# Kernel tuning notes

Measured on AMD Instinct MI355X. Metric: run time of the kernel, lower is better.

The kernel has to match this reference:

```python
import jax, jax.numpy as jnp
import numpy as np


def setup_inputs() -> dict:
    key = jax.random.key(0)
    ks = jax.random.split(key, 5)
    B, S, D_IN, D_OUT, NB, R = 4, 2048, 4096, 4096, 16, 64
    bi, bo = D_IN // NB, D_OUT // NB  # 256, 256
    x = jax.random.normal(ks[0], (B, S, D_IN), dtype=jnp.float32)
    blocks = jax.random.normal(ks[1], (NB, bo, bi), dtype=jnp.float32) * 0.02
    U = jax.random.normal(ks[2], (D_OUT, R), dtype=jnp.float32) * 0.02
    V = jax.random.normal(ks[3], (D_IN, R), dtype=jnp.float32) * 0.02
    bias = jax.random.normal(ks[4], (D_OUT,), dtype=jnp.float32)
    alpha = jnp.ones((1,), dtype=jnp.float32)
    return {"x": x, "blocks": blocks, "U": U, "V": V, "bias": bias, "alpha": alpha}


def reference(x, blocks, U, V, bias, alpha):
    # y = BlockDiag(W) x + U V^T x, scaled by alpha, plus bias.
    NB, bo, bi = blocks.shape
    batch_dims = x.shape[:-1]
    in_features = x.shape[-1]
    out_features = NB * bo
    x_flat = x.reshape(-1, in_features)                 # [N, D_in]
    x_blk = x_flat.reshape(-1, NB, bi)                  # [N, nb, bi]
    # block-diagonal: per-block GEMM with block.T, batched over blocks
    y_blk = jnp.einsum('nbi,boi->nbo', x_blk, blocks)   # [N, nb, bo]
    y_blockdiag = y_blk.reshape(-1, out_features)       # [N, D_out]
    # low-rank global term: (x V) U^T
    y_lowrank = (x_flat @ V) @ U.T                      # [N, D_out]
    result = (y_blockdiag + y_lowrank) * alpha + bias
    return result.reshape(*batch_dims, out_features)
```

## Files before the change

### kernel.cpp

```cpp
#include <hip/hip_runtime.h>
#include <hip/hip_bf16.h>


typedef __attribute__((ext_vector_type(8))) short short8;
typedef __attribute__((ext_vector_type(4))) float f32x4;

#define DIN 4096
#define DOUT 4096
#define KCAT 320

static __device__ __forceinline__ short f2bf(float f) {
  return __builtin_bit_cast(short, __float2bfloat16(f));
}
static __device__ __forceinline__ unsigned short f2bfu(float f) {
  return __builtin_bit_cast(unsigned short, __float2bfloat16(f));
}
static __device__ __forceinline__ short8 pack8(f32x4 a, f32x4 b) {
  short8 r;
  r[0] = f2bf(a[0]); r[1] = f2bf(a[1]); r[2] = f2bf(a[2]); r[3] = f2bf(a[3]);
  r[4] = f2bf(b[0]); r[5] = f2bf(b[1]); r[6] = f2bf(b[2]); r[7] = f2bf(b[3]);
  return r;
}
static __device__ __forceinline__ void gload_lds16(const void* g, void* l) {
  __builtin_amdgcn_global_load_lds(
      (const __attribute__((address_space(1))) unsigned int*)g,
      (__attribute__((address_space(3))) unsigned int*)l, 16, 0, 0);
}

__global__ __launch_bounds__(256) void prep_kernel(
    const float* __restrict__ blocks, const float* __restrict__ U,
    const float* __restrict__ V, unsigned short* __restrict__ Bmat,
    unsigned short* __restrict__ VT) {
  int g = blockIdx.x * 256 + threadIdx.x;
  const int total1 = DOUT * KCAT;
  if (g < total1) {
    int o = g / KCAT;
    int k = g - o * KCAT;
    float v;
    if (k < 256)
      v = blocks[((o >> 8) << 16) | ((o & 255) << 8) | k];
    else
      v = U[o * 64 + (k - 256)];
    Bmat[g] = f2bfu(v);
  } else {
    int g2 = g - total1;
    if (g2 < 64 * DIN) {
      int r = g2 >> 12;
      int i = g2 & (DIN - 1);
      VT[g2] = f2bfu(V[i * 64 + r]);
    }
  }
}

__global__ __launch_bounds__(256) void k1_xv(const float* __restrict__ x,
                                             const unsigned short* __restrict__ VT,
                                             float* __restrict__ tpart, int nrows) {
  const int rt = blockIdx.x >> 2;
  const int kc = blockIdx.x & 3;
  const int tid = threadIdx.x;
  const int w = tid >> 6, l = tid & 63;
  const int r0 = rt * 64 + w * 16;
  const int ko = (l >> 4) << 3;
  f32x4 acc[4];
#pragma unroll
  for (int i = 0; i < 4; ++i) acc[i] = (f32x4){0.f, 0.f, 0.f, 0.f};
  const float* xp = x + (size_t)(r0 + (l & 15)) * DIN + kc * 1024 + ko;
  const unsigned short* vp[4];
#pragma unroll
  for (int ct = 0; ct < 4; ++ct)
    vp[ct] = VT + (size_t)(ct * 16 + (l & 15)) * DIN + kc * 1024 + ko;
#pragma unroll 4
  for (int k = 0; k < 1024; k += 32) {
    f32x4 v0 = *(const f32x4*)(xp + k);
    f32x4 v1 = *(const f32x4*)(xp + k + 4);
    short8 af = pack8(v0, v1);
#pragma unroll
    for (int ct = 0; ct < 4; ++ct) {
      short8 bf = *(const short8*)(vp[ct] + k);
      acc[ct] = __builtin_amdgcn_mfma_f32_16x16x32_bf16(af, bf, acc[ct], 0, 0, 0);
    }
  }
  float* tp = tpart + (size_t)kc * nrows * 64;
  const int orow = r0 + ((l >> 4) << 2);
  const int ocol = l & 15;
#pragma unroll
  for (int ct = 0; ct < 4; ++ct)
#pragma unroll
    for (int r = 0; r < 4; ++r)
      tp[(size_t)(orow + r) * 64 + ct * 16 + ocol] = acc[ct][r];
}

__global__ __launch_bounds__(256) void k1_reduce(const float* __restrict__ tpart,
                                                 float* __restrict__ tfin, int n4) {
  int i = blockIdx.x * 256 + threadIdx.x;
  if (i >= n4) return;
  const f32x4* p = (const f32x4*)tpart;
  f32x4 s = p[i] + p[i + n4] + p[i + 2 * n4] + p[i + 3 * n4];
  ((f32x4*)tfin)[i] = s;
}

__global__ __launch_bounds__(256, 3) void k2_main(
    const float* __restrict__ x, const float* __restrict__ tfin,
    const unsigned short* __restrict__ Bmat, const float* __restrict__ bias,
    const float* __restrict__ alphap, float* __restrict__ out, int nrt) {
  __shared__ __align__(1024) float ldsA[128 * 64];
  __shared__ __align__(1024) unsigned short ldsB[128 * 64];
  const int NCT = DOUT / 128;
  const int nwg = nrt * NCT;
  const int cpx = nwg >> 3;
  const int id = blockIdx.x;
  const int sw = (id & 7) * cpx + (id >> 3);
  const int rt = sw / NCT;
  const int ct = sw - rt * NCT;
  const int row0 = rt * 128, col0 = ct * 128;
  const int b = ct >> 1;
  const int tid = threadIdx.x;
  const int w = tid >> 6, l = tid & 63;
  const int wm = w >> 1, wn = w & 1;

  int offX[8], offT[8];
#pragma unroll
  for (int r2 = 0; r2 < 8; ++r2) {
    int seg = r2 * 4 + w;
    int row = seg * 4 + (l >> 4);
    int chunk = (l & 15) >> 1;
    int half = l & 1;
    int col = (((chunk ^ (row & 7)) << 3) | (((half ^ (row >> 3)) & 1) << 2));
    offX[r2] = row * DIN + col;
    offT[r2] = row * 64 + col;
  }
  size_t offB[4];
#pragma unroll
  for (int r2 = 0; r2 < 4; ++r2) {
    int seg = r2 * 4 + w;
    int n = seg * 8 + (l >> 3);
    int kk = ((l & 7) ^ (n & 7)) << 3;
    offB[r2] = (size_t)(col0 + n) * KCAT + kk;
  }
  const float* xbase = x + (size_t)row0 * DIN + b * 256;
  const float* tbase = tfin + (size_t)row0 * 64;

  f32x4 acc[4][4];
#pragma unroll
  for (int mi = 0; mi < 4; ++mi)
#pragma unroll
    for (int ni = 0; ni < 4; ++ni) acc[mi][ni] = (f32x4){0.f, 0.f, 0.f, 0.f};

  char* ldsAb = (char*)ldsA;
  char* ldsBb = (char*)ldsB;
#pragma unroll
  for (int step = 0; step < 5; ++step) {
#pragma unroll
    for (int r2 = 0; r2 < 8; ++r2) {
      const float* src = (step < 4) ? (xbase + step * 64 + offX[r2]) : (tbase + offT[r2]);
      gload_lds16(src, ldsAb + (r2 * 4 + w) * 1024);
    }
#pragma unroll
    for (int r2 = 0; r2 < 4; ++r2)
      gload_lds16(Bmat + offB[r2] + step * 64, ldsBb + (r2 * 4 + w) * 1024);
    asm volatile("s_waitcnt vmcnt(0)" ::: "memory");
    __syncthreads();
#pragma unroll
    for (int ks = 0; ks < 2; ++ks) {
      short8 af[4], bfr[4];
#pragma unroll
      for (int mi = 0; mi < 4; ++mi) {
        int row = wm * 64 + mi * 16 + (l & 15);
        int kc2 = ks * 4 + (l >> 4);
        int off = row * 256 + (((kc2 ^ (row & 7)) << 5) | (((row >> 3) & 1) << 4));
        f32x4 v0 = *(const f32x4*)(ldsAb + off);
        f32x4 v1 = *(const f32x4*)(ldsAb + (off ^ 16));
        af[mi] = pack8(v0, v1);
      }
#pragma unroll
      for (int ni = 0; ni < 4; ++ni) {
        int n = wn * 64 + ni * 16 + (l & 15);
        int kc2 = ks * 4 + (l >> 4);
        int off = n * 128 + ((kc2 ^ (n & 7)) << 4);
        bfr[ni] = *(const short8*)(ldsBb + off);
      }
#pragma unroll
      for (int mi = 0; mi < 4; ++mi)
#pragma unroll
        for (int ni = 0; ni < 4; ++ni)
          acc[mi][ni] =
              __builtin_amdgcn_mfma_f32_16x16x32_bf16(af[mi], bfr[ni], acc[mi][ni], 0, 0, 0);
    }
    __syncthreads();
  }
  const float alpha = alphap[0];
#pragma unroll
  for (int ni = 0; ni < 4; ++ni) {
    int col = col0 + wn * 64 + ni * 16 + (l & 15);
    float bs = bias[col];
#pragma unroll
    for (int mi = 0; mi < 4; ++mi) {
      int rbase = row0 + wm * 64 + mi * 16 + ((l >> 4) << 2);
#pragma unroll
      for (int r = 0; r < 4; ++r)
        out[(size_t)(rbase + r) * DOUT + col] = acc[mi][ni][r] * alpha + bs;
    }
  }
}

extern "C" void kernel_launch(void* const* d_in, const int* in_sizes, int n_in,
                              void* d_out, int out_size, void* d_ws, size_t ws_size,
                              hipStream_t stream) {
  const float* x      = (const float*)d_in[0];
  const float* blocks = (const float*)d_in[1];
  const float* U      = (const float*)d_in[2];
  const float* V      = (const float*)d_in[3];
  const float* bias   = (const float*)d_in[4];
  const float* alpha  = (const float*)d_in[5];
  float* out = (float*)d_out;
  const int nrows = in_sizes[0] / DIN;

  char* ws = (char*)d_ws;
  float* tpart = (float*)ws;
  float* tfin  = (float*)(ws + (size_t)4 * nrows * 64 * 4);
  unsigned short* Bmat =
      (unsigned short*)(ws + (size_t)5 * nrows * 64 * 4);
  unsigned short* VT =
      (unsigned short*)(ws + (size_t)5 * nrows * 64 * 4 + (size_t)DOUT * KCAT * 2);

  const int prep_blocks = (DOUT * KCAT + 64 * DIN + 255) / 256;
  prep_kernel<<<prep_blocks, 256, 0, stream>>>(blocks, U, V, Bmat, VT);
  k1_xv<<<(nrows / 64) * 4, 256, 0, stream>>>(x, VT, tpart, nrows);
  k1_reduce<<<(nrows * 64 / 4 + 255) / 256, 256, 0, stream>>>(tpart, tfin, nrows * 64 / 4);
  k2_main<<<(nrows / 128) * (DOUT / 128), 256, 0, stream>>>(x, tfin, Bmat, bias, alpha, out,
                                                            nrows / 128);
}
```

Baseline: 301.9 us.

## Double-buffer k2_main tiles and convert A to bf16 before LDS staging

Restructures the main GEMM loop into a two-stage software pipeline: the next step's B tile is fetched via global_load_lds and the next A tile into registers while the current step's MFMAs run. A is converted from fp32 to bf16 in registers before being written to LDS, which halves A's LDS footprint and removes the per-fragment conversion in the compute loop. The cost is more registers for the prefetched A values, which is why the launch bound drops to 2 waves per SIMD, lowering occupancy.

Measured after the change: 307.6 us. No clear change (+1.9%).

```diff
diff --git a/kernel.cpp b/kernel.cpp
--- a/kernel.cpp
+++ b/kernel.cpp
@@ -99,12 +99,12 @@
   ((f32x4*)tfin)[i] = s;
 }
 
-__global__ __launch_bounds__(256, 3) void k2_main(
+__global__ __launch_bounds__(256, 2) void k2_main(
     const float* __restrict__ x, const float* __restrict__ tfin,
     const unsigned short* __restrict__ Bmat, const float* __restrict__ bias,
     const float* __restrict__ alphap, float* __restrict__ out, int nrt) {
-  __shared__ __align__(1024) float ldsA[128 * 64];
-  __shared__ __align__(1024) unsigned short ldsB[128 * 64];
+  __shared__ __align__(1024) unsigned short ldsA[2][128 * 64];
+  __shared__ __align__(1024) unsigned short ldsB[2][128 * 64];
   const int NCT = DOUT / 128;
   const int nwg = nrt * NCT;
   const int cpx = nwg >> 3;
@@ -118,27 +118,19 @@
   const int w = tid >> 6, l = tid & 63;
   const int wm = w >> 1, wn = w & 1;
 
-  int offX[8], offT[8];
-#pragma unroll
-  for (int r2 = 0; r2 < 8; ++r2) {
-    int seg = r2 * 4 + w;
-    int row = seg * 4 + (l >> 4);
-    int chunk = (l & 15) >> 1;
-    int half = l & 1;
-    int col = (((chunk ^ (row & 7)) << 3) | (((half ^ (row >> 3)) & 1) << 2));
-    offX[r2] = row * DIN + col;
-    offT[r2] = row * 64 + col;
-  }
-  size_t offB[4];
+  const int rA = tid >> 3;
+  const int c8 = tid & 7;
+
+  int offB[4];
 #pragma unroll
   for (int r2 = 0; r2 < 4; ++r2) {
     int seg = r2 * 4 + w;
     int n = seg * 8 + (l >> 3);
     int kk = ((l & 7) ^ (n & 7)) << 3;
-    offB[r2] = (size_t)(col0 + n) * KCAT + kk;
-  }
-  const float* xbase = x + (size_t)row0 * DIN + b * 256;
-  const float* tbase = tfin + (size_t)row0 * 64;
+    offB[r2] = (col0 + n) * KCAT + kk;
+  }
+  const float* xcb = x + (size_t)row0 * DIN + b * 256;
+  const float* tb = tfin + (size_t)row0 * 64;
 
   f32x4 acc[4][4];
 #pragma unroll
@@ -146,48 +138,78 @@
 #pragma unroll
     for (int ni = 0; ni < 4; ++ni) acc[mi][ni] = (f32x4){0.f, 0.f, 0.f, 0.f};
 
-  char* ldsAb = (char*)ldsA;
-  char* ldsBb = (char*)ldsB;
-#pragma unroll
-  for (int step = 0; step < 5; ++step) {
-#pragma unroll
-    for (int r2 = 0; r2 < 8; ++r2) {
-      const float* src = (step < 4) ? (xbase + step * 64 + offX[r2]) : (tbase + offT[r2]);
-      gload_lds16(src, ldsAb + (r2 * 4 + w) * 1024);
-    }
-#pragma unroll
-    for (int r2 = 0; r2 < 4; ++r2)
-      gload_lds16(Bmat + offB[r2] + step * 64, ldsBb + (r2 * 4 + w) * 1024);
+  f32x4 a0[4], a1[4];
+  char* ldsAc = (char*)&ldsA[0][0];
+  char* ldsBc = (char*)&ldsB[0][0];
+
+#define ISSUE_A(s)                                                              \
+  {                                                                             \
+    _Pragma("unroll") for (int q = 0; q < 4; ++q) {                             \
+      const float* src = ((s) < 4)                                              \
+          ? (xcb + (size_t)(q * 32 + rA) * DIN + (s) * 64 + c8 * 8)             \
+          : (tb + (q * 32 + rA) * 64 + c8 * 8);                                 \
+      a0[q] = *(const f32x4*)src;                                               \
+      a1[q] = *(const f32x4*)(src + 4);                                         \
+    }                                                                           \
+  }
+#define ISSUE_B(s, buf)                                                         \
+  {                                                                             \
+    _Pragma("unroll") for (int r2 = 0; r2 < 4; ++r2)                            \
+        gload_lds16(Bmat + offB[r2] + (s) * 64,                                 \
+                    ldsBc + (buf) * 16384 + (r2 * 4 + w) * 1024);               \
+  }
+#define WRITE_A(buf)                                                            \
+  {                                                                             \
+    _Pragma("unroll") for (int q = 0; q < 4; ++q) {                             \
+      int row = q * 32 + rA;                                                    \
+      short8 p = pack8(a0[q], a1[q]);                                           \
+      *(short8*)(ldsAc + (buf) * 16384 + row * 128 + ((c8 ^ (row & 7)) << 4)) = \
+          p;                                                                    \
+    }                                                                           \
+  }
+#define COMPUTE(buf)                                                            \
+  {                                                                             \
+    _Pragma("unroll") for (int ks = 0; ks < 2; ++ks) {                          \
+      short8 af[4], bfr[4];                                                     \
+      _Pragma("unroll") for (int mi = 0; mi < 4; ++mi) {                        \
+        int row = wm * 64 + mi * 16 + (l & 15);                                 \
+        int u = (ks * 4 + (l >> 4)) ^ (row & 7);                                \
+        af[mi] = *(const short8*)(ldsAc + (buf) * 16384 + row * 128 + (u << 4));\
+      }                                                                         \
+      _Pragma("unroll") for (int ni = 0; ni < 4; ++ni) {                        \
+        int n = wn * 64 + ni * 16 + (l & 15);                                   \
+        int u = (ks * 4 + (l >> 4)) ^ (n & 7);                                  \
+        bfr[ni] = *(const short8*)(ldsBc + (buf) * 16384 + n * 128 + (u << 4)); \
+      }                                                                         \
+      _Pragma("unroll") for (int mi = 0; mi < 4; ++mi)                          \
+          _Pragma("unroll") for (int ni = 0; ni < 4; ++ni)                      \
+              acc[mi][ni] = __builtin_amdgcn_mfma_f32_16x16x32_bf16(            \
+                  af[mi], bfr[ni], acc[mi][ni], 0, 0, 0);                       \
+    }                                                                           \
+  }
+
+  ISSUE_B(0, 0);
+  ISSUE_A(0);
+  WRITE_A(0);
+  asm volatile("s_waitcnt vmcnt(0)" ::: "memory");
+  __syncthreads();
+
+#pragma unroll
+  for (int s = 0; s < 5; ++s) {
+    const int buf = s & 1;
+    if (s < 4) {
+      ISSUE_B(s + 1, buf ^ 1);
+      ISSUE_A(s + 1);
+    }
+    COMPUTE(buf);
+    if (s < 4) {
+      __builtin_amdgcn_sched_barrier(0);
+      WRITE_A(buf ^ 1);
+    }
     asm volatile("s_waitcnt vmcnt(0)" ::: "memory");
     __syncthreads();
-#pragma unroll
-    for (int ks = 0; ks < 2; ++ks) {
-      short8 af[4], bfr[4];
-#pragma unroll
-      for (int mi = 0; mi < 4; ++mi) {
-        int row = wm * 64 + mi * 16 + (l & 15);
-        int kc2 = ks * 4 + (l >> 4);
-        int off = row * 256 + (((kc2 ^ (row & 7)) << 5) | (((row >> 3) & 1) << 4));
-        f32x4 v0 = *(const f32x4*)(ldsAb + off);
-        f32x4 v1 = *(const f32x4*)(ldsAb + (off ^ 16));
-        af[mi] = pack8(v0, v1);
-      }
-#pragma unroll
-      for (int ni = 0; ni < 4; ++ni) {
-        int n = wn * 64 + ni * 16 + (l & 15);
-        int kc2 = ks * 4 + (l >> 4);
-        int off = n * 128 + ((kc2 ^ (n & 7)) << 4);
-        bfr[ni] = *(const short8*)(ldsBb + off);
-      }
-#pragma unroll
-      for (int mi = 0; mi < 4; ++mi)
-#pragma unroll
-        for (int ni = 0; ni < 4; ++ni)
-          acc[mi][ni] =
-              __builtin_amdgcn_mfma_f32_16x16x32_bf16(af[mi], bfr[ni], acc[mi][ni], 0, 0, 0);
-    }
-    __syncthreads();
-  }
+  }
+
   const float alpha = alphap[0];
 #pragma unroll
   for (int ni = 0; ni < 4; ++ni) {
@@ -201,6 +223,10 @@
         out[(size_t)(rbase + r) * DOUT + col] = acc[mi][ni][r] * alpha + bs;
     }
   }
+#undef ISSUE_A
+#undef ISSUE_B
+#undef WRITE_A
+#undef COMPUTE
 }
 
 extern "C" void kernel_launch(void* const* d_in, const int* in_sizes, int n_in,
```

## Load A operand directly from global, double-buffer B in LDS, fuse partial reduction

Applied to the files above, without the earlier changes.

Removes the k1_reduce kernel and instead sums the four split-K partials of x·V inside k2_main when forming the low-rank A fragment. The A operand (x and t) is now read straight from global memory into registers per wave rather than staged through LDS, while the B operand uses a double-buffered LDS scheme so the next step's load overlaps current MFMAs. This saves one launch and LDS traffic for A, but each wave now issues uncoalesced-ish direct global loads whose latency is not hidden, and the t partials get re-read by every column tile.

Measured after the change: 389.9 us. 29.1% more time.

```diff
diff --git a/kernel.cpp b/kernel.cpp
--- a/kernel.cpp
+++ b/kernel.cpp
@@ -90,21 +90,11 @@
       tp[(size_t)(orow + r) * 64 + ct * 16 + ocol] = acc[ct][r];
 }
 
-__global__ __launch_bounds__(256) void k1_reduce(const float* __restrict__ tpart,
-                                                 float* __restrict__ tfin, int n4) {
-  int i = blockIdx.x * 256 + threadIdx.x;
-  if (i >= n4) return;
-  const f32x4* p = (const f32x4*)tpart;
-  f32x4 s = p[i] + p[i + n4] + p[i + 2 * n4] + p[i + 3 * n4];
-  ((f32x4*)tfin)[i] = s;
-}
-
 __global__ __launch_bounds__(256, 3) void k2_main(
-    const float* __restrict__ x, const float* __restrict__ tfin,
+    const float* __restrict__ x, const float* __restrict__ tpart,
     const unsigned short* __restrict__ Bmat, const float* __restrict__ bias,
-    const float* __restrict__ alphap, float* __restrict__ out, int nrt) {
-  __shared__ __align__(1024) float ldsA[128 * 64];
-  __shared__ __align__(1024) unsigned short ldsB[128 * 64];
+    const float* __restrict__ alphap, float* __restrict__ out, int nrt, int nrows) {
+  __shared__ __align__(1024) unsigned short ldsB[2][128 * 64];
   const int NCT = DOUT / 128;
   const int nwg = nrt * NCT;
   const int cpx = nwg >> 3;
@@ -117,28 +107,25 @@
   const int tid = threadIdx.x;
   const int w = tid >> 6, l = tid & 63;
   const int wm = w >> 1, wn = w & 1;
-
-  int offX[8], offT[8];
-#pragma unroll
-  for (int r2 = 0; r2 < 8; ++r2) {
-    int seg = r2 * 4 + w;
-    int row = seg * 4 + (l >> 4);
-    int chunk = (l & 15) >> 1;
-    int half = l & 1;
-    int col = (((chunk ^ (row & 7)) << 3) | (((half ^ (row >> 3)) & 1) << 2));
-    offX[r2] = row * DIN + col;
-    offT[r2] = row * 64 + col;
-  }
-  size_t offB[4];
+  const int lr = l & 15, lk = l >> 4;
+
+  int offB[4];
 #pragma unroll
   for (int r2 = 0; r2 < 4; ++r2) {
     int seg = r2 * 4 + w;
     int n = seg * 8 + (l >> 3);
     int kk = ((l & 7) ^ (n & 7)) << 3;
-    offB[r2] = (size_t)(col0 + n) * KCAT + kk;
-  }
-  const float* xbase = x + (size_t)row0 * DIN + b * 256;
-  const float* tbase = tfin + (size_t)row0 * 64;
+    offB[r2] = (col0 + n) * KCAT + kk;
+  }
+  const float* xrow[4];
+  const float* trow[4];
+  const size_t kcs = (size_t)nrows * 64;
+#pragma unroll
+  for (int mi = 0; mi < 4; ++mi) {
+    int grow = row0 + wm * 64 + mi * 16 + lr;
+    xrow[mi] = x + (size_t)grow * DIN + b * 256 + lk * 8;
+    trow[mi] = tpart + (size_t)grow * 64 + lk * 8;
+  }
 
   f32x4 acc[4][4];
 #pragma unroll
@@ -146,38 +133,49 @@
 #pragma unroll
     for (int ni = 0; ni < 4; ++ni) acc[mi][ni] = (f32x4){0.f, 0.f, 0.f, 0.f};
 
-  char* ldsAb = (char*)ldsA;
-  char* ldsBb = (char*)ldsB;
-#pragma unroll
-  for (int step = 0; step < 5; ++step) {
-#pragma unroll
-    for (int r2 = 0; r2 < 8; ++r2) {
-      const float* src = (step < 4) ? (xbase + step * 64 + offX[r2]) : (tbase + offT[r2]);
-      gload_lds16(src, ldsAb + (r2 * 4 + w) * 1024);
-    }
-#pragma unroll
-    for (int r2 = 0; r2 < 4; ++r2)
-      gload_lds16(Bmat + offB[r2] + step * 64, ldsBb + (r2 * 4 + w) * 1024);
-    asm volatile("s_waitcnt vmcnt(0)" ::: "memory");
-    __syncthreads();
+  char* ldsBc = (char*)&ldsB[0][0];
+#pragma unroll
+  for (int r2 = 0; r2 < 4; ++r2)
+    gload_lds16(Bmat + offB[r2], ldsBc + (r2 * 4 + w) * 1024);
+  asm volatile("s_waitcnt vmcnt(0)" ::: "memory");
+  __syncthreads();
+
+#pragma unroll
+  for (int s = 0; s < 5; ++s) {
+    const int buf = s & 1;
+    if (s < 4) {
+#pragma unroll
+      for (int r2 = 0; r2 < 4; ++r2)
+        gload_lds16(Bmat + offB[r2] + (s + 1) * 64,
+                    ldsBc + (buf ^ 1) * 16384 + (r2 * 4 + w) * 1024);
+    }
 #pragma unroll
     for (int ks = 0; ks < 2; ++ks) {
       short8 af[4], bfr[4];
 #pragma unroll
       for (int mi = 0; mi < 4; ++mi) {
-        int row = wm * 64 + mi * 16 + (l & 15);
-        int kc2 = ks * 4 + (l >> 4);
-        int off = row * 256 + (((kc2 ^ (row & 7)) << 5) | (((row >> 3) & 1) << 4));
-        f32x4 v0 = *(const f32x4*)(ldsAb + off);
-        f32x4 v1 = *(const f32x4*)(ldsAb + (off ^ 16));
-        af[mi] = pack8(v0, v1);
+        f32x4 lo, hi;
+        if (s < 4) {
+          const float* p = xrow[mi] + s * 64 + ks * 32;
+          lo = *(const f32x4*)p;
+          hi = *(const f32x4*)(p + 4);
+        } else {
+          const float* p = trow[mi] + ks * 32;
+          lo = *(const f32x4*)p;
+          hi = *(const f32x4*)(p + 4);
+#pragma unroll
+          for (int kc = 1; kc < 4; ++kc) {
+            lo += *(const f32x4*)(p + kc * kcs);
+            hi += *(const f32x4*)(p + kc * kcs + 4);
+          }
+        }
+        af[mi] = pack8(lo, hi);
       }
 #pragma unroll
       for (int ni = 0; ni < 4; ++ni) {
-        int n = wn * 64 + ni * 16 + (l & 15);
-        int kc2 = ks * 4 + (l >> 4);
-        int off = n * 128 + ((kc2 ^ (n & 7)) << 4);
-        bfr[ni] = *(const short8*)(ldsBb + off);
+        int n = wn * 64 + ni * 16 + lr;
+        int u = (ks * 4 + lk) ^ (n & 7);
+        bfr[ni] = *(const short8*)(ldsBc + buf * 16384 + n * 128 + (u << 4));
       }
 #pragma unroll
       for (int mi = 0; mi < 4; ++mi)
@@ -186,16 +184,18 @@
           acc[mi][ni] =
               __builtin_amdgcn_mfma_f32_16x16x32_bf16(af[mi], bfr[ni], acc[mi][ni], 0, 0, 0);
     }
+    asm volatile("s_waitcnt vmcnt(0)" ::: "memory");
     __syncthreads();
   }
+
   const float alpha = alphap[0];
 #pragma unroll
   for (int ni = 0; ni < 4; ++ni) {
-    int col = col0 + wn * 64 + ni * 16 + (l & 15);
+    int col = col0 + wn * 64 + ni * 16 + lr;
     float bs = bias[col];
 #pragma unroll
     for (int mi = 0; mi < 4; ++mi) {
-      int rbase = row0 + wm * 64 + mi * 16 + ((l >> 4) << 2);
+      int rbase = row0 + wm * 64 + mi * 16 + (lk << 2);
 #pragma unroll
       for (int r = 0; r < 4; ++r)
         out[(size_t)(rbase + r) * DOUT + col] = acc[mi][ni][r] * alpha + bs;
@@ -217,16 +217,14 @@
 
   char* ws = (char*)d_ws;
   float* tpart = (float*)ws;
-  float* tfin  = (float*)(ws + (size_t)4 * nrows * 64 * 4);
   unsigned short* Bmat =
-      (unsigned short*)(ws + (size_t)5 * nrows * 64 * 4);
+      (unsigned short*)(ws + (size_t)4 * nrows * 64 * 4);
   unsigned short* VT =
-      (unsigned short*)(ws + (size_t)5 * nrows * 64 * 4 + (size_t)DOUT * KCAT * 2);
+      (unsigned short*)(ws + (size_t)4 * nrows * 64 * 4 + (size_t)DOUT * KCAT * 2);
 
   const int prep_blocks = (DOUT * KCAT + 64 * DIN + 255) / 256;
   prep_kernel<<<prep_blocks, 256, 0, stream>>>(blocks, U, V, Bmat, VT);
   k1_xv<<<(nrows / 64) * 4, 256, 0, stream>>>(x, VT, tpart, nrows);
-  k1_reduce<<<(nrows * 64 / 4 + 255) / 256, 256, 0, stream>>>(tpart, tfin, nrows * 64 / 4);
-  k2_main<<<(nrows / 128) * (DOUT / 128), 256, 0, stream>>>(x, tfin, Bmat, bias, alpha, out,
-                                                            nrows / 128);
-}
+  k2_main<<<(nrows / 128) * (DOUT / 128), 256, 0, stream>>>(x, tpart, Bmat, bias, alpha, out,
+                                                            nrows / 128, nrows);
+}
```
